# Kernel optimization log

Hardware: AMD Instinct MI355X
Metric: run time of the kernel (lower is better)

The kernel has to match this reference:

```python
import jax, jax.numpy as jnp
import numpy as np

D = 512; H = 8; DFF = 2048; S1 = 1024; S2 = 512; B = 8; EPS = 1e-5


def setup_inputs() -> dict:
    key = jax.random.key(0)
    ks = jax.random.split(key, 10)
    def w(k, shape):
        return jax.random.normal(k, shape, dtype=jnp.float32) * 0.02
    return {
        "rna_embed": jax.random.normal(ks[0], (S1, B, D), dtype=jnp.float32),
        "protein_embed": jax.random.normal(ks[1], (S2, B, D), dtype=jnp.float32),
        # self-attention params (torch MHA packed in_proj)
        "Wqkv_s": w(ks[2], (3 * D, D)), "bqkv_s": jnp.zeros((3 * D,), jnp.float32),
        "Wo_s": w(ks[3], (D, D)), "bo_s": jnp.zeros((D,), jnp.float32),
        # cross-attention params
        "Wqkv_c": w(ks[4], (3 * D, D)), "bqkv_c": jnp.zeros((3 * D,), jnp.float32),
        "Wo_c": w(ks[5], (D, D)), "bo_c": jnp.zeros((D,), jnp.float32),
        # FFN params
        "W1": w(ks[6], (DFF, D)), "b1": jnp.zeros((DFF,), jnp.float32),
        "W2": w(ks[7], (D, DFF)), "b2": jnp.zeros((D,), jnp.float32),
        # LayerNorm params: norm0_1, norm1_1, norm1_2, norm2
        "g0": jnp.ones((D,), jnp.float32), "be0": jnp.zeros((D,), jnp.float32),
        "g11": jnp.ones((D,), jnp.float32), "be11": jnp.zeros((D,), jnp.float32),
        "g12": jnp.ones((D,), jnp.float32), "be12": jnp.zeros((D,), jnp.float32),
        "g2": jnp.ones((D,), jnp.float32), "be2": jnp.zeros((D,), jnp.float32),
    }


def _layernorm(x, g, b):
    m = jnp.mean(x, axis=-1, keepdims=True)
    v = jnp.mean(jnp.square(x - m), axis=-1, keepdims=True)
    return (x - m) * jax.lax.rsqrt(v + EPS) * g + b


def _mha(xq, xkv, Wqkv, bqkv, Wo, bo):
    # xq: (Sq, B, D), xkv: (Sk, B, D)
    Wq, Wk, Wv = jnp.split(Wqkv, 3, axis=0)
    bq, bk, bv = jnp.split(bqkv, 3)
    hd = D // H
    scale = 1.0 / np.sqrt(hd).astype(np.float32)
    q = (xq @ Wq.T + bq).reshape(xq.shape[0], -1, H, hd)   # (Sq,B,H,hd)
    k = (xkv @ Wk.T + bk).reshape(xkv.shape[0], -1, H, hd)  # (Sk,B,H,hd)
    v = (xkv @ Wv.T + bv).reshape(xkv.shape[0], -1, H, hd)
    scores = jnp.einsum('qbhd,kbhd->bhqk', q, k) * scale    # (B,H,Sq,Sk)
    attn = jax.nn.softmax(scores, axis=-1)
    o = jnp.einsum('bhqk,kbhd->qbhd', attn, v).reshape(xq.shape[0], -1, D)
    return o @ Wo.T + bo


def reference(rna_embed, protein_embed, Wqkv_s, bqkv_s, Wo_s, bo_s,
              Wqkv_c, bqkv_c, Wo_c, bo_c, W1, b1, W2, b2,
              g0, be0, g11, be11, g12, be12, g2, be2):
    x1 = rna_embed
    # pre-norm self-attention
    h = _layernorm(x1, g0, be0)
    x1 = x1 + _mha(h, h, Wqkv_s, bqkv_s, Wo_s, bo_s)
    # pre-norm cross-attention (queries from x1, keys/values from protein)
    x1 = x1 + _mha(_layernorm(x1, g11, be11), _layernorm(protein_embed, g12, be12),
                   Wqkv_c, bqkv_c, Wo_c, bo_c)
    # pre-norm FFN
    h = _layernorm(x1, g2, be2)
    x1 = x1 + (jax.nn.relu(h @ W1.T + b1) @ W2.T + b2)
    return x1
```

## Files before the change

### kernel.cpp

```cpp
#include <hip/hip_runtime.h>

typedef unsigned short u16;
typedef unsigned int u32;
typedef u16 u16x8 __attribute__((ext_vector_type(8)));
typedef u16 u16x4 __attribute__((ext_vector_type(4)));
typedef short bfx8 __attribute__((ext_vector_type(8)));
typedef float f32x4 __attribute__((ext_vector_type(4)));

#define AS1 __attribute__((address_space(1)))
#define AS3 __attribute__((address_space(3)))

__device__ __forceinline__ u16 f2bf(float f) {
  union { float f; u32 u; } c; c.f = f;
  u32 u = c.u;
  u += 0x7fffu + ((u >> 16) & 1u);
  return (u16)(u >> 16);
}

__device__ __forceinline__ float bf2f(u16 b) {
  union { u32 u; float f; } c; c.u = ((u32)b) << 16;
  return c.f;
}

__device__ __forceinline__ u32 cvt_pk_bf16(float lo, float hi) {
  u32 r;
  asm("v_cvt_pk_bf16_f32 %0, %1, %2" : "=v"(r) : "v"(lo), "v"(hi));
  return r;
}

__device__ __forceinline__ float fexp2(float x) {
  float r;
  asm("v_exp_f32 %0, %1" : "=v"(r) : "v"(x));
  return r;
}

__device__ __forceinline__ void ln_core(float f[8], const float* __restrict__ g,
                                        const float* __restrict__ be,
                                        u16* __restrict__ out, int gw, int lane) {
  float s = 0.f, q = 0.f;
#pragma unroll
  for (int e = 0; e < 8; ++e) { s += f[e]; q += f[e] * f[e]; }
#pragma unroll
  for (int m = 1; m < 64; m <<= 1) { s += __shfl_xor(s, m); q += __shfl_xor(q, m); }
  float mean = s * (1.f / 512.f);
  float var = q * (1.f / 512.f) - mean * mean;
  float rs = rsqrtf(var + 1e-5f);
  const float4* g4 = (const float4*)g;
  const float4* b4 = (const float4*)be;
  float4 ga = g4[2 * lane], gb = g4[2 * lane + 1];
  float4 ba = b4[2 * lane], bb = b4[2 * lane + 1];
  float gv[8] = {ga.x, ga.y, ga.z, ga.w, gb.x, gb.y, gb.z, gb.w};
  float bv[8] = {ba.x, ba.y, ba.z, ba.w, bb.x, bb.y, bb.z, bb.w};
  u16x8 o;
#pragma unroll
  for (int e = 0; e < 8; ++e) o[e] = f2bf((f[e] - mean) * rs * gv[e] + bv[e]);
  ((u16x8*)(out + (size_t)gw * 512))[lane] = o;
}

__device__ __forceinline__ void ln_row_f32(const float* __restrict__ x, const float* __restrict__ g,
                                           const float* __restrict__ be, u16* __restrict__ out,
                                           int gw, int lane) {
  const float4* row = (const float4*)(x + (size_t)gw * 512);
  float4 a = row[2 * lane], b = row[2 * lane + 1];
  float f[8] = {a.x, a.y, a.z, a.w, b.x, b.y, b.z, b.w};
  ln_core(f, g, be, out, gw, lane);
}

__device__ __forceinline__ void ln_row_bf16(const u16* __restrict__ x, const float* __restrict__ g,
                                            const float* __restrict__ be, u16* __restrict__ out,
                                            int gw, int lane) {
  u16x8 v = ((const u16x8*)(x + (size_t)gw * 512))[lane];
  float f[8];
#pragma unroll
  for (int e = 0; e < 8; ++e) f[e] = bf2f(v[e]);
  ln_core(f, g, be, out, gw, lane);
}

__global__ __launch_bounds__(256) void cvtln_kernel(const float* __restrict__ a0, const float* __restrict__ a1,
                                                    const float* __restrict__ a2, const float* __restrict__ a3,
                                                    const float* __restrict__ a4, const float* __restrict__ a5,
                                                    u16* __restrict__ b0, u16* __restrict__ b1,
                                                    u16* __restrict__ b2, u16* __restrict__ b3,
                                                    u16* __restrict__ b4, u16* __restrict__ b5,
                                                    const float* __restrict__ x, const float* __restrict__ g,
                                                    const float* __restrict__ be, u16* __restrict__ lnout,
                                                    const float* __restrict__ xp, const float* __restrict__ gp,
                                                    const float* __restrict__ bep, u16* __restrict__ lnoutp) {
  if (blockIdx.x < 4096) {
    int i = blockIdx.x * 256 + threadIdx.x;
    const float* s; u16* d; int off;
    if      (i < 196608) { s = a0; d = b0; off = i; }
    else if (i < 262144) { s = a1; d = b1; off = i - 196608; }
    else if (i < 458752) { s = a2; d = b2; off = i - 262144; }
    else if (i < 524288) { s = a3; d = b3; off = i - 458752; }
    else if (i < 786432) { s = a4; d = b4; off = i - 524288; }
    else                 { s = a5; d = b5; off = i - 786432; }
    float4 v = ((const float4*)s)[off];
    u16x4 o;
    o[0] = f2bf(v.x); o[1] = f2bf(v.y); o[2] = f2bf(v.z); o[3] = f2bf(v.w);
    ((u16x4*)d)[off] = o;
  } else if (blockIdx.x < 6144) {
    int gw = ((blockIdx.x - 4096) * 256 + threadIdx.x) >> 6;
    ln_row_f32(x, g, be, lnout, gw, threadIdx.x & 63);
  } else {
    int gw = ((blockIdx.x - 6144) * 256 + threadIdx.x) >> 6;
    ln_row_f32(xp, gp, bep, lnoutp, gw, threadIdx.x & 63);
  }
}

__global__ __launch_bounds__(256) void lnb_kernel(const u16* __restrict__ x,
                                                  const float* __restrict__ g,
                                                  const float* __restrict__ be,
                                                  u16* __restrict__ out, int ntok) {
  int gw = (blockIdx.x * 256 + threadIdx.x) >> 6;
  if (gw >= ntok) return;
  ln_row_bf16(x, g, be, out, gw, threadIdx.x & 63);
}

__device__ __forceinline__ void vt_body(const u16* __restrict__ vB, u16* __restrict__ vt,
                                        int stride, int S, int xblk, int b, int h) {
  __shared__ u16 lt[64 * 68];
  const int t = threadIdx.x;
  const int sr = t >> 3, dc = (t & 7) * 8;
#pragma unroll
  for (int p = 0; p < 2; ++p) {
    int s = xblk * 64 + sr + p * 32;
    u16x8 v = *(const u16x8*)(vB + (size_t)(s * 8 + b) * stride + h * 64 + dc);
    u16x4 lo, hi;
    lo[0]=v[0]; lo[1]=v[1]; lo[2]=v[2]; lo[3]=v[3];
    hi[0]=v[4]; hi[1]=v[5]; hi[2]=v[6]; hi[3]=v[7];
    *(u16x4*)&lt[(sr + p * 32) * 68 + dc] = lo;
    *(u16x4*)&lt[(sr + p * 32) * 68 + dc + 4] = hi;
  }
  __syncthreads();
#pragma unroll
  for (int p = 0; p < 2; ++p) {
    int d = sr + p * 32;
    u16x8 o;
#pragma unroll
    for (int e = 0; e < 8; ++e) o[e] = lt[(dc + e) * 68 + d];
    *(u16x8*)(vt + ((size_t)(b * 8 + h) * 64 + d) * S + xblk * 64 + dc) = o;
  }
}

__global__ __launch_bounds__(256) void vt2_kernel(const u16* __restrict__ v0, u16* __restrict__ t0,
                                                  const u16* __restrict__ v1, u16* __restrict__ t1) {
  int id = blockIdx.x;
  if (id < 1024) {
    vt_body(v0, t0, 1536, 1024, id & 15, (id >> 4) & 7, id >> 7);
  } else {
    int l = id - 1024;
    vt_body(v1, t1, 1024, 512, l & 7, (l >> 3) & 7, l >> 6);
  }
}

template <int EPI, int BM, int BN, int WRg>
__device__ __forceinline__ void gemm8_body(const u16* __restrict__ A,
                                           const u16* __restrict__ Bw,
                                           const float* __restrict__ bias,
                                           const void* __restrict__ res,
                                           void* __restrict__ Cout,
                                           int M, int K, int bn, int bm,
                                           u16* __restrict__ lds) {
  constexpr int WCg = 8 / WRg;
  constexpr int RPW = BM / WRg;
  constexpr int IM = RPW / 16;
  constexpr int CPW = BN / WCg;
  constexpr int JN = CPW / 16;
  constexpr int LD = (BM + BN) / 64;
  u16* lA = lds;
  u16* lB = lds + 2 * BM * 64;
  const int tid = threadIdx.x;
  const int lane = tid & 63, w = tid >> 6;
  const int wr = w / WCg, wc = w % WCg;
  const int r15 = lane & 15, kg = lane >> 4;
  const int xr = (r15 & 7) << 4;

  f32x4 acc[IM][JN] = {};

  const int lrw = tid >> 3;
  const int lcl = ((tid & 7) * 8) ^ ((lrw & 7) * 8);
  const u16* gA = A + (size_t)(bn + lrw) * K + lcl;
  const u16* gB = Bw + (size_t)(bm + lrw) * K + lcl;
  const int ldsbase = (w * 8) * 64;

#define STAGE8(buf, t) do {                                                               \
    _Pragma("unroll")                                                                     \
    for (int i_ = 0; i_ < BM / 64; ++i_)                                                  \
      __builtin_amdgcn_global_load_lds((AS1 u32*)(gA + (size_t)(i_ * 64) * K + (t) * 64), \
                                       (AS3 u32*)&lA[(buf) * BM * 64 + i_ * 4096 + ldsbase], 16, 0, 0);\
    _Pragma("unroll")                                                                     \
    for (int i_ = 0; i_ < BN / 64; ++i_)                                                  \
      __builtin_amdgcn_global_load_lds((AS1 u32*)(gB + (size_t)(i_ * 64) * K + (t) * 64), \
                                       (AS3 u32*)&lB[(buf) * BN * 64 + i_ * 4096 + ldsbase], 16, 0, 0);\
  } while (0)

  const int nk = K >> 6;
  STAGE8(0, 0);
  for (int t = 0; t < nk; ++t) {
    const int cur = t & 1;
    if (t + 1 < nk) {
      STAGE8(cur ^ 1, t + 1);
      if constexpr (LD == 3)      asm volatile("s_waitcnt vmcnt(3)" ::: "memory");
      else if constexpr (LD == 4) asm volatile("s_waitcnt vmcnt(4)" ::: "memory");
      else                        asm volatile("s_waitcnt vmcnt(8)" ::: "memory");
    } else {
      asm volatile("s_waitcnt vmcnt(0)" ::: "memory");
    }
    __builtin_amdgcn_sched_barrier(0);
    __builtin_amdgcn_s_barrier();
    __builtin_amdgcn_sched_barrier(0);

    const char* Ac = (const char*)&lA[cur * BM * 64];
    const char* Bc = (const char*)&lB[cur * BN * 64];
    __builtin_amdgcn_s_setprio(1);
#pragma unroll
    for (int kk = 0; kk < 2; ++kk) {
      bfx8 a[IM], b[JN];
#pragma unroll
      for (int i = 0; i < IM; ++i)
        a[i] = *(const bfx8*)(Ac + (wr * RPW + i * 16 + r15) * 128 + ((kk * 64 + kg * 16) ^ xr));
#pragma unroll
      for (int j = 0; j < JN; ++j)
        b[j] = *(const bfx8*)(Bc + (wc * CPW + j * 16 + r15) * 128 + ((kk * 64 + kg * 16) ^ xr));
#pragma unroll
      for (int i = 0; i < IM; ++i)
#pragma unroll
        for (int j = 0; j < JN; ++j)
          acc[i][j] = __builtin_amdgcn_mfma_f32_16x16x32_bf16(a[i], b[j], acc[i][j], 0, 0, 0);
    }
    __builtin_amdgcn_s_setprio(0);
    __builtin_amdgcn_sched_barrier(0);
    __builtin_amdgcn_s_barrier();
  }
#undef STAGE8

#pragma unroll
  for (int i = 0; i < IM; ++i) {
#pragma unroll
    for (int j = 0; j < JN; ++j) {
      int col = bm + wc * CPW + j * 16 + r15;
      float bv = bias[col];
#pragma unroll
      for (int r = 0; r < 4; ++r) {
        int row = bn + wr * RPW + i * 16 + kg * 4 + r;
        size_t idx = (size_t)row * M + col;
        float v = acc[i][j][r] + bv;
        if (EPI == 1) v = fmaxf(v, 0.f);
        if (EPI == 3) {
          ((u16*)Cout)[idx] = f2bf(((const float*)res)[idx] + v);
        } else if (EPI == 4) {
          ((u16*)Cout)[idx] = f2bf(bf2f(((const u16*)res)[idx]) + v);
        } else if (EPI == 5) {
          ((float*)Cout)[idx] = bf2f(((const u16*)res)[idx]) + v;
        } else {
          ((u16*)Cout)[idx] = f2bf(v);
        }
      }
    }
  }
}

template <int EPI, int BM, int BN, int WRg, int MINW>
__global__ __launch_bounds__(512, MINW) void gemm8(const u16* __restrict__ A,
                                                   const u16* __restrict__ Bw,
                                                   const float* __restrict__ bias,
                                                   const void* __restrict__ res,
                                                   void* __restrict__ Cout,
                                                   int N, int M, int K) {
  __shared__ __align__(16) u16 lds[2 * (BM + BN) * 64];
  const int nwg = gridDim.x * gridDim.y;
  const int id = blockIdx.y * gridDim.x + blockIdx.x;
  const int swz = (id & 7) * (nwg >> 3) + (id >> 3);
  const int bn = (swz / gridDim.x) * BM;
  const int bm = (swz % gridDim.x) * BN;
  gemm8_body<EPI, BM, BN, WRg>(A, Bw, bias, res, Cout, M, K, bn, bm, lds);
}

__global__ __launch_bounds__(512, 4) void gemm_qkvkv(const u16* __restrict__ A0, const u16* __restrict__ W0,
                                                     const float* __restrict__ c0, u16* __restrict__ O0,
                                                     const u16* __restrict__ A1, const u16* __restrict__ W1,
                                                     const float* __restrict__ c1, u16* __restrict__ O1) {
  __shared__ __align__(16) u16 lds[2 * 256 * 64];
  const int id = blockIdx.x;
  if (id < 768) {
    const int swz = (id & 7) * 96 + (id >> 3);
    gemm8_body<0, 128, 128, 4>(A0, W0, c0, nullptr, O0, 1536, 512,
                               (swz / 12) * 128, (swz % 12) * 128, lds);
  } else {
    const int lid = id - 768;
    const int swz = (lid & 7) * 64 + (lid >> 3);
    gemm8_body<0, 64, 128, 2>(A1, W1, c1, nullptr, O1, 1024, 512,
                              (swz / 8) * 64, (swz % 8) * 128, lds);
  }
}

__global__ __launch_bounds__(256, 2) void attn_kernel(const u16* __restrict__ qB,
                                                      const u16* __restrict__ kB,
                                                      const u16* __restrict__ vtB,
                                                      u16* __restrict__ oB,
                                                      int qStride, int kvStride, int Sk) {
  __shared__ __align__(16) u16 lK[4][64 * 64];
  __shared__ __align__(16) u16 lVt[4][64 * 64];
  const int tid = threadIdx.x, lane = tid & 63, w = tid >> 6;
  const int sid = blockIdx.x;
  const int h = sid & 7, b = (sid >> 3) & 7, qt = sid >> 6;
  const int r15 = lane & 15, kg = lane >> 4;
  const int srow = lane >> 3;
  const int sxcol = ((lane & 7) * 8) ^ (srow * 8);

  const int q0 = qt * 128 + w * 32 + r15;
  const u16* qrow0 = qB + (size_t)(q0 * 8 + b) * qStride + h * 64;
  const u16* qrow1 = qB + (size_t)((q0 + 16) * 8 + b) * qStride + h * 64;
  bfx8 qf0a = *(const bfx8*)(qrow0 + kg * 8);
  bfx8 qf0b = *(const bfx8*)(qrow0 + 32 + kg * 8);
  bfx8 qf1a = *(const bfx8*)(qrow1 + kg * 8);
  bfx8 qf1b = *(const bfx8*)(qrow1 + 32 + kg * 8);

  const int rlA = w * 16 + srow;
  const int rlB = rlA + 8;
  const int krA = (rlA & 32) | ((rlA & 12) << 1) | ((rlA & 16) >> 2) | (rlA & 3);
  const int krB = (rlB & 32) | ((rlB & 12) << 1) | ((rlB & 16) >> 2) | (rlB & 3);

  const u16* vbase = vtB + ((size_t)(b * 8 + h) * 64) * Sk;
  const u16* kpA = kB + ((size_t)krA * 8 + b) * kvStride + h * 64 + sxcol;
  const u16* kpB = kB + ((size_t)krB * 8 + b) * kvStride + h * 64 + sxcol;
  const size_t kAdv = (size_t)64 * 8 * kvStride;
  const u16* vpA = vbase + (size_t)rlA * Sk + sxcol;
  const u16* vpB = vbase + (size_t)rlB * Sk + sxcol;

#define STAGE(buf, tt) do {                                                           \
    __builtin_amdgcn_global_load_lds((AS1 u32*)(kpA + (size_t)(tt) * kAdv),           \
                                     (AS3 u32*)&lK[buf][(w * 16) * 64], 16, 0, 0);    \
    __builtin_amdgcn_global_load_lds((AS1 u32*)(kpB + (size_t)(tt) * kAdv),           \
                                     (AS3 u32*)&lK[buf][(w * 16 + 8) * 64], 16, 0, 0);\
    __builtin_amdgcn_global_load_lds((AS1 u32*)(vpA + (size_t)(tt) * 64),             \
                                     (AS3 u32*)&lVt[buf][(w * 16) * 64], 16, 0, 0);   \
    __builtin_amdgcn_global_load_lds((AS1 u32*)(vpB + (size_t)(tt) * 64),             \
                                     (AS3 u32*)&lVt[buf][(w * 16 + 8) * 64], 16, 0, 0);\
  } while (0)

  const int nt = Sk / 64;
  const int np = nt >> 1;
  STAGE(0, 0); STAGE(1, 1);

  f32x4 oacc0[4] = {}, oacc1[4] = {};
  float mrow0 = -1e30f, mrow1 = -1e30f, lsum0 = 0.f, lsum1 = 0.f;
  const float C2 = 0.125f * 1.44269504088896340736f;
  const int xr = (r15 & 7) << 4;

  for (int i = 0; i < np; ++i) {
    __builtin_amdgcn_sched_barrier(0);
    __builtin_amdgcn_s_barrier();
    __builtin_amdgcn_sched_barrier(0);
    if (i + 1 < np) {
      const int sb = ((i + 1) & 1) * 2;
      STAGE(sb, 2 * (i + 1)); STAGE(sb + 1, 2 * (i + 1) + 1);
      asm volatile("s_waitcnt vmcnt(8)" ::: "memory");
    } else {
      asm volatile("s_waitcnt vmcnt(0)" ::: "memory");
    }
    __builtin_amdgcn_sched_barrier(0);

#pragma unroll
    for (int tb = 0; tb < 2; ++tb) {
      const int buf = (i & 1) * 2 + tb;
      const char* Kc = (const char*)lK[buf];
      const char* Vc = (const char*)lVt[buf];

      f32x4 s0[4] = {}, s1[4] = {};
      __builtin_amdgcn_s_setprio(1);
#pragma unroll
      for (int j = 0; j < 4; ++j) {
        const char* kp = Kc + (j * 16 + r15) * 128;
        bfx8 kf0 = *(const bfx8*)(kp + ((kg * 16) ^ xr));
        bfx8 kf1 = *(const bfx8*)(kp + ((64 + kg * 16) ^ xr));
        s0[j] = __builtin_amdgcn_mfma_f32_16x16x32_bf16(kf0, qf0a, s0[j], 0, 0, 0);
        s0[j] = __builtin_amdgcn_mfma_f32_16x16x32_bf16(kf1, qf0b, s0[j], 0, 0, 0);
        s1[j] = __builtin_amdgcn_mfma_f32_16x16x32_bf16(kf0, qf1a, s1[j], 0, 0, 0);
        s1[j] = __builtin_amdgcn_mfma_f32_16x16x32_bf16(kf1, qf1b, s1[j], 0, 0, 0);
      }
      __builtin_amdgcn_s_setprio(0);

      float lm0 = fmaxf(fmaxf(fmaxf(s0[0][0], s0[0][1]), fmaxf(s0[0][2], s0[0][3])),
                 fmaxf(fmaxf(fmaxf(s0[1][0], s0[1][1]), fmaxf(s0[1][2], s0[1][3])),
                 fmaxf(fmaxf(fmaxf(s0[2][0], s0[2][1]), fmaxf(s0[2][2], s0[2][3])),
                       fmaxf(fmaxf(s0[3][0], s0[3][1]), fmaxf(s0[3][2], s0[3][3])))));
      if (!__all(lm0 <= mrow0 + 16.0f)) {
        float m0 = fmaxf(lm0, __shfl_xor(lm0, 16));
        m0 = fmaxf(m0, __shfl_xor(m0, 32));
        float mn = fmaxf(mrow0, m0);
        float corr = fexp2((mrow0 - mn) * C2);
        mrow0 = mn;
        lsum0 *= corr;
#pragma unroll
        for (int jd = 0; jd < 4; ++jd)
#pragma unroll
          for (int r = 0; r < 4; ++r) oacc0[jd][r] *= corr;
      }
      float lm1 = fmaxf(fmaxf(fmaxf(s1[0][0], s1[0][1]), fmaxf(s1[0][2], s1[0][3])),
                 fmaxf(fmaxf(fmaxf(s1[1][0], s1[1][1]), fmaxf(s1[1][2], s1[1][3])),
                 fmaxf(fmaxf(fmaxf(s1[2][0], s1[2][1]), fmaxf(s1[2][2], s1[2][3])),
                       fmaxf(fmaxf(s1[3][0], s1[3][1]), fmaxf(s1[3][2], s1[3][3])))));
      if (!__all(lm1 <= mrow1 + 16.0f)) {
        float m1 = fmaxf(lm1, __shfl_xor(lm1, 16));
        m1 = fmaxf(m1, __shfl_xor(m1, 32));
        float mn = fmaxf(mrow1, m1);
        float corr = fexp2((mrow1 - mn) * C2);
        mrow1 = mn;
        lsum1 *= corr;
#pragma unroll
        for (int jd = 0; jd < 4; ++jd)
#pragma unroll
          for (int r = 0; r < 4; ++r) oacc1[jd][r] *= corr;
      }

      float bc0 = -mrow0 * C2, bc1 = -mrow1 * C2;
      float p0[4][4], p1[4][4];
      float ps0 = 0.f, ps1 = 0.f;
#pragma unroll
      for (int j = 0; j < 4; ++j)
#pragma unroll
        for (int r = 0; r < 4; ++r) {
          p0[j][r] = fexp2(fmaf(s0[j][r], C2, bc0));
          p1[j][r] = fexp2(fmaf(s1[j][r], C2, bc1));
          ps0 += p0[j][r]; ps1 += p1[j][r];
        }
      lsum0 += ps0; lsum1 += ps1;

      __builtin_amdgcn_s_setprio(1);
#pragma unroll
      for (int s2 = 0; s2 < 2; ++s2) {
        union { u32 u[4]; bfx8 v; } pt0, pt1;
        pt0.u[0] = cvt_pk_bf16(p0[2 * s2][0],     p0[2 * s2][1]);
        pt0.u[1] = cvt_pk_bf16(p0[2 * s2][2],     p0[2 * s2][3]);
        pt0.u[2] = cvt_pk_bf16(p0[2 * s2 + 1][0], p0[2 * s2 + 1][1]);
        pt0.u[3] = cvt_pk_bf16(p0[2 * s2 + 1][2], p0[2 * s2 + 1][3]);
        pt1.u[0] = cvt_pk_bf16(p1[2 * s2][0],     p1[2 * s2][1]);
        pt1.u[1] = cvt_pk_bf16(p1[2 * s2][2],     p1[2 * s2][3]);
        pt1.u[2] = cvt_pk_bf16(p1[2 * s2 + 1][0], p1[2 * s2 + 1][1]);
        pt1.u[3] = cvt_pk_bf16(p1[2 * s2 + 1][2], p1[2 * s2 + 1][3]);
#pragma unroll
        for (int jd = 0; jd < 4; ++jd) {
          const char* vp = Vc + (jd * 16 + r15) * 128;
          bfx8 vf = *(const bfx8*)(vp + ((s2 * 64 + kg * 16) ^ xr));
          oacc0[jd] = __builtin_amdgcn_mfma_f32_16x16x32_bf16(vf, pt0.v, oacc0[jd], 0, 0, 0);
          oacc1[jd] = __builtin_amdgcn_mfma_f32_16x16x32_bf16(vf, pt1.v, oacc1[jd], 0, 0, 0);
        }
      }
      __builtin_amdgcn_s_setprio(0);
    }
  }
#undef STAGE

  lsum0 += __shfl_xor(lsum0, 16);
  lsum0 += __shfl_xor(lsum0, 32);
  lsum1 += __shfl_xor(lsum1, 16);
  lsum1 += __shfl_xor(lsum1, 32);
  float inv0 = 1.f / lsum0, inv1 = 1.f / lsum1;
  u16* orow0 = oB + (size_t)(q0 * 8 + b) * 512 + h * 64;
  u16* orow1 = oB + (size_t)((q0 + 16) * 8 + b) * 512 + h * 64;
#pragma unroll
  for (int jd = 0; jd < 4; ++jd) {
    *(u32*)(orow0 + jd * 16 + kg * 4)     = cvt_pk_bf16(oacc0[jd][0] * inv0, oacc0[jd][1] * inv0);
    *(u32*)(orow0 + jd * 16 + kg * 4 + 2) = cvt_pk_bf16(oacc0[jd][2] * inv0, oacc0[jd][3] * inv0);
    *(u32*)(orow1 + jd * 16 + kg * 4)     = cvt_pk_bf16(oacc1[jd][0] * inv1, oacc1[jd][1] * inv1);
    *(u32*)(orow1 + jd * 16 + kg * 4 + 2) = cvt_pk_bf16(oacc1[jd][2] * inv1, oacc1[jd][3] * inv1);
  }
}

extern "C" void kernel_launch(void* const* d_in, const int* in_sizes, int n_in,
                              void* d_out, int out_size, void* d_ws, size_t ws_size,
                              hipStream_t stream) {
  const float* rna    = (const float*)d_in[0];
  const float* prot   = (const float*)d_in[1];
  const float* Wqkv_s = (const float*)d_in[2];
  const float* bqkv_s = (const float*)d_in[3];
  const float* Wo_s   = (const float*)d_in[4];
  const float* bo_s   = (const float*)d_in[5];
  const float* Wqkv_c = (const float*)d_in[6];
  const float* bqkv_c = (const float*)d_in[7];
  const float* Wo_c   = (const float*)d_in[8];
  const float* bo_c   = (const float*)d_in[9];
  const float* W1     = (const float*)d_in[10];
  const float* b1     = (const float*)d_in[11];
  const float* W2     = (const float*)d_in[12];
  const float* b2     = (const float*)d_in[13];
  const float* g0  = (const float*)d_in[14];
  const float* be0 = (const float*)d_in[15];
  const float* g11 = (const float*)d_in[16];
  const float* be11= (const float*)d_in[17];
  const float* g12 = (const float*)d_in[18];
  const float* be12= (const float*)d_in[19];
  const float* g2  = (const float*)d_in[20];
  const float* be2 = (const float*)d_in[21];
  float* out = (float*)d_out;

  u16* wbf      = (u16*)d_ws;
  u16* w_qkv_s  = wbf;
  u16* w_o_s    = wbf + 786432;
  u16* w_qkv_c  = wbf + 1048576;
  u16* w_o_c    = wbf + 1835008;
  u16* w_1      = wbf + 2097152;
  u16* w_2      = wbf + 3145728;
  u16* hbuf     = wbf + 4194304;
  u16* qkv      = hbuf + 4194304;
  u16* kvc      = qkv + 4194304;
  u16* attnO    = qkv + 12582912;
  u16* hp       = attnO + 4194304;
  u16* x1b      = hp + 2097152;
  u16* x1c      = x1b + 4194304;
  u16* ffnmid   = qkv;

  cvtln_kernel<<<7168, 256, 0, stream>>>(Wqkv_s, Wo_s, Wqkv_c, Wo_c, W1, W2,
                                         w_qkv_s, w_o_s, w_qkv_c, w_o_c, w_1, w_2,
                                         rna, g0, be0, hbuf, prot, g12, be12, hp);

  gemm_qkvkv<<<1280, 512, 0, stream>>>(hbuf, w_qkv_s, bqkv_s, qkv,
                                       hp, w_qkv_c + 512 * 512, bqkv_c + 512, kvc);

  vt2_kernel<<<1536, 256, 0, stream>>>(qkv + 1024, hbuf, kvc + 512, hp);

  attn_kernel<<<512, 256, 0, stream>>>(qkv, qkv + 512, hbuf, attnO, 1536, 1536, 1024);
  gemm8<3, 64, 128, 2, 6><<<dim3(4, 128), 512, 0, stream>>>(attnO, w_o_s, bo_s, rna, x1b, 8192, 512, 512);

  lnb_kernel<<<2048, 256, 0, stream>>>(x1b, g11, be11, hbuf, 8192);
  gemm8<0, 64, 128, 2, 6><<<dim3(4, 128), 512, 0, stream>>>(hbuf, w_qkv_c, bqkv_c, nullptr, qkv, 8192, 512, 512);
  attn_kernel<<<512, 256, 0, stream>>>(qkv, kvc, hp, attnO, 512, 1024, 512);
  gemm8<4, 64, 128, 2, 6><<<dim3(4, 128), 512, 0, stream>>>(attnO, w_o_c, bo_c, x1b, x1c, 8192, 512, 512);

  lnb_kernel<<<2048, 256, 0, stream>>>(x1c, g2, be2, hbuf, 8192);
  gemm8<1, 128, 128, 4, 4><<<dim3(16, 64), 512, 0, stream>>>(hbuf, w_1, b1, nullptr, ffnmid, 8192, 2048, 512);
  gemm8<5, 64, 128, 2, 6><<<dim3(4, 128), 512, 0, stream>>>(ffnmid, w_2, b2, x1c, out, 8192, 512, 2048);
}
```

Measured before the change: 174.0 us.

## Fold LayerNorm into following GEMMs via gamma-scaled weights and epilogue stats

Removes the two standalone bf16 LayerNorm kernels before the cross-attention Q projection and the FFN up-projection. LayerNorm gamma is folded into the bf16 weights during conversion, and the column sums of W*gamma and W*beta are precomputed. Row mean and variance are accumulated from the A fragments inside the GEMM main loop and applied in the epilogue. This saves two launches and a full activation read/write round trip each, at the cost of extra ALU work in the GEMM inner loop and a one-pass variance (E[x^2]-mean^2) that is less numerically robust.

```diff
diff --git a/kernel.cpp b/kernel.cpp
--- a/kernel.cpp
+++ b/kernel.cpp
@@ -66,16 +66,6 @@
   ln_core(f, g, be, out, gw, lane);
 }
 
-__device__ __forceinline__ void ln_row_bf16(const u16* __restrict__ x, const float* __restrict__ g,
-                                            const float* __restrict__ be, u16* __restrict__ out,
-                                            int gw, int lane) {
-  u16x8 v = ((const u16x8*)(x + (size_t)gw * 512))[lane];
-  float f[8];
-#pragma unroll
-  for (int e = 0; e < 8; ++e) f[e] = bf2f(v[e]);
-  ln_core(f, g, be, out, gw, lane);
-}
-
 __global__ __launch_bounds__(256) void cvtln_kernel(const float* __restrict__ a0, const float* __restrict__ a1,
                                                     const float* __restrict__ a2, const float* __restrict__ a3,
                                                     const float* __restrict__ a4, const float* __restrict__ a5,
@@ -85,36 +75,55 @@
                                                     const float* __restrict__ x, const float* __restrict__ g,
                                                     const float* __restrict__ be, u16* __restrict__ lnout,
                                                     const float* __restrict__ xp, const float* __restrict__ gp,
-                                                    const float* __restrict__ bep, u16* __restrict__ lnoutp) {
+                                                    const float* __restrict__ bep, u16* __restrict__ lnoutp,
+                                                    const float* __restrict__ g11, const float* __restrict__ be11,
+                                                    const float* __restrict__ g2, const float* __restrict__ be2,
+                                                    float* __restrict__ s_qc, float* __restrict__ badd_qc,
+                                                    float* __restrict__ s_f1, float* __restrict__ badd_f1) {
   if (blockIdx.x < 4096) {
     int i = blockIdx.x * 256 + threadIdx.x;
-    const float* s; u16* d; int off;
+    const float* s; u16* d; int off; int fold = 0;
     if      (i < 196608) { s = a0; d = b0; off = i; }
     else if (i < 262144) { s = a1; d = b1; off = i - 196608; }
-    else if (i < 458752) { s = a2; d = b2; off = i - 262144; }
+    else if (i < 458752) { s = a2; d = b2; off = i - 262144; fold = (off < 65536) ? 1 : 0; }
     else if (i < 524288) { s = a3; d = b3; off = i - 458752; }
-    else if (i < 786432) { s = a4; d = b4; off = i - 524288; }
+    else if (i < 786432) { s = a4; d = b4; off = i - 524288; fold = 2; }
     else                 { s = a5; d = b5; off = i - 786432; }
     float4 v = ((const float4*)s)[off];
+    if (fold) {
+      const float* gf = (fold == 1) ? g11 : g2;
+      int base = (off * 4) & 511;
+      v.x *= gf[base]; v.y *= gf[base + 1]; v.z *= gf[base + 2]; v.w *= gf[base + 3];
+    }
     u16x4 o;
     o[0] = f2bf(v.x); o[1] = f2bf(v.y); o[2] = f2bf(v.z); o[3] = f2bf(v.w);
     ((u16x4*)d)[off] = o;
   } else if (blockIdx.x < 6144) {
     int gw = ((blockIdx.x - 4096) * 256 + threadIdx.x) >> 6;
     ln_row_f32(x, g, be, lnout, gw, threadIdx.x & 63);
-  } else {
+  } else if (blockIdx.x < 7168) {
     int gw = ((blockIdx.x - 6144) * 256 + threadIdx.x) >> 6;
     ln_row_f32(xp, gp, bep, lnoutp, gw, threadIdx.x & 63);
-  }
-}
-
-__global__ __launch_bounds__(256) void lnb_kernel(const u16* __restrict__ x,
-                                                  const float* __restrict__ g,
-                                                  const float* __restrict__ be,
-                                                  u16* __restrict__ out, int ntok) {
-  int gw = (blockIdx.x * 256 + threadIdx.x) >> 6;
-  if (gw >= ntok) return;
-  ln_row_bf16(x, g, be, out, gw, threadIdx.x & 63);
+  } else {
+    int wv = (blockIdx.x - 7168) * 4 + (threadIdx.x >> 6);
+    if (wv >= 2560) return;
+    int lane = threadIdx.x & 63;
+    const float* W; const float* gm; const float* bt; float* so; float* bo; int c;
+    if (wv < 512) { W = a2; gm = g11; bt = be11; so = s_qc; bo = badd_qc; c = wv; }
+    else          { W = a4; gm = g2;  bt = be2;  so = s_f1; bo = badd_f1; c = wv - 512; }
+    const float* row = W + (size_t)c * 512 + lane * 8;
+    float sv = 0.f, bv = 0.f;
+#pragma unroll
+    for (int e = 0; e < 8; ++e) {
+      int k = lane * 8 + e;
+      float wvl = row[e];
+      sv = fmaf(gm[k], wvl, sv);
+      bv = fmaf(bt[k], wvl, bv);
+    }
+#pragma unroll
+    for (int m = 1; m < 64; m <<= 1) { sv += __shfl_xor(sv, m); bv += __shfl_xor(bv, m); }
+    if (lane == 0) { so[c] = sv; bo[c] = bv; }
+  }
 }
 
 __device__ __forceinline__ void vt_body(const u16* __restrict__ vB, u16* __restrict__ vt,
@@ -161,7 +170,10 @@
                                            const void* __restrict__ res,
                                            void* __restrict__ Cout,
                                            int M, int K, int bn, int bm,
-                                           u16* __restrict__ lds) {
+                                           u16* __restrict__ lds,
+                                           const float* __restrict__ scol = nullptr,
+                                           const float* __restrict__ badd = nullptr) {
+  constexpr bool LNA = (EPI == 8 || EPI == 9);
   constexpr int WCg = 8 / WRg;
   constexpr int RPW = BM / WRg;
   constexpr int IM = RPW / 16;
@@ -170,6 +182,7 @@
   constexpr int LD = (BM + BN) / 64;
   u16* lA = lds;
   u16* lB = lds + 2 * BM * 64;
+  float2* statsL = (float2*)lds;
   const int tid = threadIdx.x;
   const int lane = tid & 63, w = tid >> 6;
   const int wr = w / WCg, wc = w % WCg;
@@ -177,6 +190,7 @@
   const int xr = (r15 & 7) << 4;
 
   f32x4 acc[IM][JN] = {};
+  float sA[IM] = {}, sQ[IM] = {};
 
   const int lrw = tid >> 3;
   const int lcl = ((tid & 7) * 8) ^ ((lrw & 7) * 8);
@@ -223,6 +237,16 @@
 #pragma unroll
       for (int j = 0; j < JN; ++j)
         b[j] = *(const bfx8*)(Bc + (wc * CPW + j * 16 + r15) * 128 + ((kk * 64 + kg * 16) ^ xr));
+      if constexpr (LNA) {
+#pragma unroll
+        for (int i = 0; i < IM; ++i)
+#pragma unroll
+          for (int e = 0; e < 8; ++e) {
+            float xv = bf2f((u16)a[i][e]);
+            sA[i] += xv;
+            sQ[i] = fmaf(xv, xv, sQ[i]);
+          }
+      }
 #pragma unroll
       for (int i = 0; i < IM; ++i)
 #pragma unroll
@@ -235,26 +259,53 @@
   }
 #undef STAGE8
 
+  if constexpr (LNA) {
+#pragma unroll
+    for (int i = 0; i < IM; ++i) {
+      sA[i] += __shfl_xor(sA[i], 16); sA[i] += __shfl_xor(sA[i], 32);
+      sQ[i] += __shfl_xor(sQ[i], 16); sQ[i] += __shfl_xor(sQ[i], 32);
+    }
+    __syncthreads();
+    if (kg == 0) {
+#pragma unroll
+      for (int i = 0; i < IM; ++i)
+        statsL[wr * RPW + i * 16 + r15] = make_float2(sA[i], sQ[i]);
+    }
+    __syncthreads();
+  }
+
 #pragma unroll
   for (int i = 0; i < IM; ++i) {
 #pragma unroll
     for (int j = 0; j < JN; ++j) {
       int col = bm + wc * CPW + j * 16 + r15;
       float bv = bias[col];
+      float sc = 0.f, ba = 0.f;
+      if (LNA) { sc = scol[col]; ba = badd[col]; }
 #pragma unroll
       for (int r = 0; r < 4; ++r) {
         int row = bn + wr * RPW + i * 16 + kg * 4 + r;
         size_t idx = (size_t)row * M + col;
-        float v = acc[i][j][r] + bv;
-        if (EPI == 1) v = fmaxf(v, 0.f);
-        if (EPI == 3) {
-          ((u16*)Cout)[idx] = f2bf(((const float*)res)[idx] + v);
-        } else if (EPI == 4) {
-          ((u16*)Cout)[idx] = f2bf(bf2f(((const u16*)res)[idx]) + v);
-        } else if (EPI == 5) {
-          ((float*)Cout)[idx] = bf2f(((const u16*)res)[idx]) + v;
+        if (EPI == 8 || EPI == 9) {
+          float2 st = statsL[row - bn];
+          float mean = st.x * (1.f / 512.f);
+          float var = st.y * (1.f / 512.f) - mean * mean;
+          float rs = rsqrtf(var + 1e-5f);
+          float o = rs * acc[i][j][r] - rs * mean * sc + bv + ba;
+          if (EPI == 9) o = fmaxf(o, 0.f);
+          ((u16*)Cout)[idx] = f2bf(o);
         } else {
-          ((u16*)Cout)[idx] = f2bf(v);
+          float v = acc[i][j][r] + bv;
+          if (EPI == 1) v = fmaxf(v, 0.f);
+          if (EPI == 3) {
+            ((u16*)Cout)[idx] = f2bf(((const float*)res)[idx] + v);
+          } else if (EPI == 4) {
+            ((u16*)Cout)[idx] = f2bf(bf2f(((const u16*)res)[idx]) + v);
+          } else if (EPI == 5) {
+            ((float*)Cout)[idx] = bf2f(((const u16*)res)[idx]) + v;
+          } else {
+            ((u16*)Cout)[idx] = f2bf(v);
+          }
         }
       }
     }
@@ -267,14 +318,16 @@
                                                    const float* __restrict__ bias,
                                                    const void* __restrict__ res,
                                                    void* __restrict__ Cout,
-                                                   int N, int M, int K) {
+                                                   int N, int M, int K,
+                                                   const float* scol = nullptr,
+                                                   const float* badd = nullptr) {
   __shared__ __align__(16) u16 lds[2 * (BM + BN) * 64];
   const int nwg = gridDim.x * gridDim.y;
   const int id = blockIdx.y * gridDim.x + blockIdx.x;
   const int swz = (id & 7) * (nwg >> 3) + (id >> 3);
   const int bn = (swz / gridDim.x) * BM;
   const int bm = (swz % gridDim.x) * BN;
-  gemm8_body<EPI, BM, BN, WRg>(A, Bw, bias, res, Cout, M, K, bn, bm, lds);
+  gemm8_body<EPI, BM, BN, WRg>(A, Bw, bias, res, Cout, M, K, bn, bm, lds, scol, badd);
 }
 
 __global__ __launch_bounds__(512, 4) void gemm_qkvkv(const u16* __restrict__ A0, const u16* __restrict__ W0,
@@ -511,10 +564,16 @@
   u16* x1b      = hp + 2097152;
   u16* x1c      = x1b + 4194304;
   u16* ffnmid   = qkv;
-
-  cvtln_kernel<<<7168, 256, 0, stream>>>(Wqkv_s, Wo_s, Wqkv_c, Wo_c, W1, W2,
+  float* s_qc    = (float*)(x1c + 4194304);
+  float* badd_qc = s_qc + 512;
+  float* s_f1    = s_qc + 1024;
+  float* badd_f1 = s_qc + 3072;
+
+  cvtln_kernel<<<7808, 256, 0, stream>>>(Wqkv_s, Wo_s, Wqkv_c, Wo_c, W1, W2,
                                          w_qkv_s, w_o_s, w_qkv_c, w_o_c, w_1, w_2,
-                                         rna, g0, be0, hbuf, prot, g12, be12, hp);
+                                         rna, g0, be0, hbuf, prot, g12, be12, hp,
+                                         g11, be11, g2, be2,
+                                         s_qc, badd_qc, s_f1, badd_f1);
 
   gemm_qkvkv<<<1280, 512, 0, stream>>>(hbuf, w_qkv_s, bqkv_s, qkv,
                                        hp, w_qkv_c + 512 * 512, bqkv_c + 512, kvc);
@@ -524,12 +583,12 @@
   attn_kernel<<<512, 256, 0, stream>>>(qkv, qkv + 512, hbuf, attnO, 1536, 1536, 1024);
   gemm8<3, 64, 128, 2, 6><<<dim3(4, 128), 512, 0, stream>>>(attnO, w_o_s, bo_s, rna, x1b, 8192, 512, 512);
 
-  lnb_kernel<<<2048, 256, 0, stream>>>(x1b, g11, be11, hbuf, 8192);
-  gemm8<0, 64, 128, 2, 6><<<dim3(4, 128), 512, 0, stream>>>(hbuf, w_qkv_c, bqkv_c, nullptr, qkv, 8192, 512, 512);
+  gemm8<8, 64, 128, 2, 6><<<dim3(4, 128), 512, 0, stream>>>(x1b, w_qkv_c, bqkv_c, nullptr, qkv,
+                                                            8192, 512, 512, s_qc, badd_qc);
   attn_kernel<<<512, 256, 0, stream>>>(qkv, kvc, hp, attnO, 512, 1024, 512);
   gemm8<4, 64, 128, 2, 6><<<dim3(4, 128), 512, 0, stream>>>(attnO, w_o_c, bo_c, x1b, x1c, 8192, 512, 512);
 
-  lnb_kernel<<<2048, 256, 0, stream>>>(x1c, g2, be2, hbuf, 8192);
-  gemm8<1, 128, 128, 4, 4><<<dim3(16, 64), 512, 0, stream>>>(hbuf, w_1, b1, nullptr, ffnmid, 8192, 2048, 512);
+  gemm8<9, 128, 128, 4, 4><<<dim3(16, 64), 512, 0, stream>>>(x1c, w_1, b1, nullptr, ffnmid,
+                                                             8192, 2048, 512, s_f1, badd_f1);
   gemm8<5, 64, 128, 2, 6><<<dim3(4, 128), 512, 0, stream>>>(ffnmid, w_2, b2, x1c, out, 8192, 512, 2048);
 }
```

Result: slower. 180.5 us (+3.7%).
